# Optimization experiments

Measured on AMD Instinct MI355X. Metric: run time of the kernel, lower is better.

## Reference

```python
import jax, jax.numpy as jnp
import numpy as np

N_NODES = 50000
N_EDGES = 1_600_000
NUM_GRAPHS = 64
F_NODE = 32
F_EDGE = 16
H = 64
L = 3
BN_EPS = 1e-5


def setup_inputs() -> dict:
    key = jax.random.key(0)
    ks = jax.random.split(key, 20)
    x = jax.random.normal(ks[0], (N_NODES, F_NODE), jnp.float32)
    edge_attr = jax.random.normal(ks[1], (N_EDGES, F_EDGE), jnp.float32)
    edge_index = jax.random.randint(ks[2], (2, N_EDGES), 0, N_NODES, dtype=jnp.int64)
    batch = jnp.sort(jax.random.randint(ks[3], (N_NODES,), 0, NUM_GRAPHS, dtype=jnp.int64))

    def lin(k, fan_in, shape):
        return jax.random.normal(k, shape, jnp.float32) * (1.0 / np.sqrt(fan_in))

    node_W = lin(ks[4], F_NODE, (F_NODE, H));  node_b = jnp.zeros((H,), jnp.float32)
    edge_W = lin(ks[5], F_EDGE, (F_EDGE, H));  edge_b = jnp.zeros((H,), jnp.float32)
    # GINE per-layer MLP: Linear(H, 2H) -> ReLU -> Linear(2H, H)
    W1s = lin(ks[6], H, (L, H, 2 * H));   b1s = jnp.zeros((L, 2 * H), jnp.float32)
    W2s = lin(ks[7], 2 * H, (L, 2 * H, H)); b2s = jnp.zeros((L, H), jnp.float32)
    gammas = jnp.ones((L, H), jnp.float32)
    betas = jnp.zeros((L, H), jnp.float32)
    lin_W = lin(ks[8], H, (H, 1));  lin_b = jnp.zeros((1,), jnp.float32)
    return {
        "x": x, "edge_attr": edge_attr, "edge_index": edge_index, "batch": batch,
        "node_W": node_W, "node_b": node_b, "edge_W": edge_W, "edge_b": edge_b,
        "W1s": W1s, "b1s": b1s, "W2s": W2s, "b2s": b2s,
        "gammas": gammas, "betas": betas, "lin_W": lin_W, "lin_b": lin_b,
    }


def reference(x, edge_attr, edge_index, batch, node_W, node_b, edge_W, edge_b,
              W1s, b1s, W2s, b2s, gammas, betas, lin_W, lin_b):
    # node / edge embeddings
    h = x @ node_W + node_b                  # [N, H]
    e = edge_attr @ edge_W + edge_b          # [E, H]
    src, dst = edge_index[0], edge_index[1]
    for l in range(L):
        # GINEConv (eps=0): m_ij = relu(x_j + e_ij), aggregate sum at target
        m = jax.nn.relu(h[src] + e)                                  # [E, H]
        agg = jax.ops.segment_sum(m, dst, num_segments=N_NODES)     # [N, H]
        z = h + agg
        z = jax.nn.relu(z @ W1s[l] + b1s[l]) @ W2s[l] + b2s[l]       # GINE MLP
        # BatchNorm (training-mode batch stats, biased variance) + ReLU
        mu = jnp.mean(z, axis=0)
        var = jnp.var(z, axis=0)
        h = jax.nn.relu(gammas[l] * (z - mu) * jax.lax.rsqrt(var + BN_EPS) + betas[l])
    # global mean pool per graph
    counts = jax.ops.segment_sum(jnp.ones((N_NODES,), h.dtype), batch, num_segments=NUM_GRAPHS)
    gsum = jax.ops.segment_sum(h, batch, num_segments=NUM_GRAPHS)   # [G, H]
    graph_x = gsum / jnp.maximum(counts, 1.0)[:, None]
    return graph_x @ lin_W + lin_b                                   # [G, 1]
```

## Files before the change

kernel.cpp:

```cpp
#include <hip/hip_runtime.h>

#define NN 50000
#define NE 1600000
#define NG 64
#define HD 64
#define BN_EPS 1e-5f
#define NTILES ((NN + 31) / 32)
#define NBUCK 8
#define NPB 6250
#define NBINS (NBUCK * NN)
#define NEP (NE + 512)
#define SLOTS 3584

typedef unsigned short ushort_t;
typedef unsigned int uint_t;
typedef __attribute__((ext_vector_type(8))) short bf16x8;
typedef __attribute__((ext_vector_type(4))) float f32x4;

__device__ __forceinline__ float b2f(ushort_t u) {
  union { uint_t i; float f; } v; v.i = ((uint_t)u) << 16; return v.f;
}
__device__ __forceinline__ ushort_t f2b(float f) {
  union { float f; uint_t i; } v; v.f = f;
  uint_t x = v.i;
  return (ushort_t)((x + 0x7fffu + ((x >> 16) & 1u)) >> 16);
}
__device__ __forceinline__ uint_t packsplit(float f) {
  ushort_t hi = f2b(f);
  float r = f - b2f(hi);
  ushort_t lo = f2b(r);
  return (uint_t)hi | ((uint_t)lo << 16);
}
__device__ __forceinline__ float LDF(const void* p, int i, int isb) {
  return isb ? b2f(((const ushort_t*)p)[i]) : ((const float*)p)[i];
}
__device__ __forceinline__ int LDI(const void* p, int i, int is64) {
  return is64 ? ((const int*)p)[2 * i] : ((const int*)p)[i];
}
__device__ __forceinline__ int clampi(int v, int hi) {
  return (v < 0) ? 0 : (v >= hi ? hi - 1 : v);
}

__global__ void detect_k(const uint_t* __restrict__ xw, const uint_t* __restrict__ ew,
                         int* __restrict__ flags) {
  int t = threadIdx.x;
  uint_t w = xw[t];
  uint_t b = (w >> 8) & 0x7fu;
  unsigned long long m1 = __ballot(b >= 0x3au && b <= 0x42u);
  unsigned long long m2 = __ballot(ew[2 * t + 1] == 0u);
  if (t == 0) {
    flags[0] = (__popcll(m1) >= 32) ? 1 : 0;
    flags[1] = (__popcll(m2) >= 56) ? 1 : 0;
  }
}

__global__ void __launch_bounds__(256) node_embed(
    const void* __restrict__ x, const void* __restrict__ W,
    const void* __restrict__ b, float* __restrict__ h, const int* __restrict__ flags) {
  __shared__ float xs[64 * 32];
  int isb = flags[0];
  int t = threadIdx.x;
  int base = blockIdx.x * 64;
  int nodes = NN - base; if (nodes > 64) nodes = 64;
  int idx = t * 8;
  if (idx < nodes * 32) {
    if (isb) {
      const uint4* p = (const uint4*)((const ushort_t*)x + base * 32);
      uint4 u = p[t];
      ushort_t* pu = (ushort_t*)&u;
      #pragma unroll
      for (int q = 0; q < 8; q++) xs[idx + q] = b2f(pu[q]);
    } else {
      const float4* p = (const float4*)((const float*)x + base * 32);
      float4 a = p[2 * t], d = p[2 * t + 1];
      xs[idx + 0] = a.x; xs[idx + 1] = a.y; xs[idx + 2] = a.z; xs[idx + 3] = a.w;
      xs[idx + 4] = d.x; xs[idx + 5] = d.y; xs[idx + 6] = d.z; xs[idx + 7] = d.w;
    }
  }
  int c = t & 63, s0 = t >> 6;
  float w[32];
  #pragma unroll
  for (int k = 0; k < 32; k++) w[k] = LDF(W, k * 64 + c, isb);
  float bc = LDF(b, c, isb);
  __syncthreads();
  #pragma unroll 4
  for (int i = 0; i < 16; i++) {
    int slot = s0 * 16 + i;
    int node = base + slot;
    if (node < NN) {
      float acc = bc;
      #pragma unroll
      for (int k = 0; k < 32; k++) acc += xs[slot * 32 + k] * w[k];
      h[node * 64 + c] = acc;
    }
  }
}

__global__ void __launch_bounds__(256) hist_k(
    const void* __restrict__ eidx, int* __restrict__ hist, const int* __restrict__ flags) {
  int is64 = flags[1];
  int e = blockIdx.x * 256 + threadIdx.x;
  if (e >= NE) return;
  int d = clampi(LDI(eidx, NE + e, is64), NN);
  int s = clampi(LDI(eidx, e, is64), NN);
  int bin = (s / NPB) * NN + d;
  atomicAdd(&hist[bin], 1);
}

__global__ void __launch_bounds__(1024) scan_k(
    const int* __restrict__ hist, int* __restrict__ starts, int* __restrict__ meta) {
  __shared__ int buf[1024];
  __shared__ int sA[NBUCK + 1];
  __shared__ int sT[NBUCK];
  __shared__ int sPT[NBUCK];
  int t = threadIdx.x;
  int active = t < 1000;
  const int4* h4 = (const int4*)hist;
  int4* s4 = (int4*)starts;
  int ssum = 0;
  if (active) {
    for (int i = t * 100; i < t * 100 + 100; i++) {
      int4 v = h4[i];
      ssum += v.x + v.y + v.z + v.w;
    }
  }
  buf[t] = ssum;
  __syncthreads();
  if (t < NBUCK) {
    int T = 0;
    for (int i = t * 125; i < t * 125 + 125; i++) T += buf[i];
    sT[t] = T;
  }
  __syncthreads();
  if (t == 0) {
    int a = 0, pt = 0;
    for (int b = 0; b < NBUCK; b++) {
      sA[b] = a; sPT[b] = pt;
      meta[b] = a;
      meta[16 + b] = a + sT[b];
      pt += sT[b];
      a = (a + sT[b] + 63) & ~63;
    }
    sA[NBUCK] = a;
    meta[NBUCK] = a;
  }
  __syncthreads();
  for (int d = 1; d < 1024; d <<= 1) {
    int x = (t >= d) ? buf[t - d] : 0;
    __syncthreads();
    buf[t] += x;
    __syncthreads();
  }
  if (active) {
    int b = t / 125;
    int run = sA[b] + (buf[t] - ssum - sPT[b]);
    for (int i = t * 100; i < t * 100 + 100; i++) {
      int4 v = h4[i];
      int4 o;
      o.x = run; run += v.x;
      o.y = run; run += v.y;
      o.z = run; run += v.z;
      o.w = run; run += v.w;
      s4[i] = o;
    }
  }
}

__global__ void pad_fill(const int* __restrict__ meta, int* __restrict__ perm,
                         int* __restrict__ psrc, int* __restrict__ pdst) {
  int t = threadIdx.x;
  for (int b = 0; b < NBUCK; b++) {
    int re = meta[16 + b], ae = meta[b + 1];
    for (int p = re + t; p < ae; p += 64) {
      perm[p] = 0; psrc[p] = 0; pdst[p] = NN;
    }
  }
}

__global__ void __launch_bounds__(256) scatter_k(
    const void* __restrict__ eidx, int* __restrict__ cursor,
    int* __restrict__ perm, int* __restrict__ psrc, int* __restrict__ pdst,
    const int* __restrict__ flags) {
  int is64 = flags[1];
  int e = blockIdx.x * 256 + threadIdx.x;
  if (e >= NE) return;
  int d = clampi(LDI(eidx, NE + e, is64), NN);
  int s = clampi(LDI(eidx, e, is64), NN);
  int bin = (s / NPB) * NN + d;
  int pos = atomicAdd(&cursor[bin], 1);
  perm[pos] = e;
  psrc[pos] = s;
  pdst[pos] = d;
}

__global__ void __launch_bounds__(256) pack_eattr(
    const void* __restrict__ eattr, const int* __restrict__ perm,
    ushort_t* __restrict__ phi, ushort_t* __restrict__ plo,
    const int* __restrict__ flags, const int* __restrict__ meta) {
  int isb = flags[0];
  int pos = blockIdx.x * 256 + threadIdx.x;
  if (pos >= meta[8]) return;
  int e = perm[pos];
  int tile = pos >> 4, r = pos & 15;
  union U8 { ushort_t s[8]; uint4 u; };
  if (isb) {
    const uint4* p = (const uint4*)((const ushort_t*)eattr + (size_t)e * 16);
    uint4 h0 = p[0], h1 = p[1];
    ((uint4*)phi)[tile * 32 + r] = h0;
    ((uint4*)phi)[tile * 32 + 16 + r] = h1;
  } else {
    const float4* p = (const float4*)((const float*)eattr + (size_t)e * 16);
    U8 hi[2], lo[2];
    #pragma unroll
    for (int q = 0; q < 4; q++) {
      float4 v = p[q];
      float vv[4] = {v.x, v.y, v.z, v.w};
      #pragma unroll
      for (int j = 0; j < 4; j++) {
        int idx = q * 4 + j;
        ushort_t hb = f2b(vv[j]);
        hi[idx >> 3].s[idx & 7] = hb;
        lo[idx >> 3].s[idx & 7] = f2b(vv[j] - b2f(hb));
      }
    }
    ((uint4*)phi)[tile * 32 + r] = hi[0].u;
    ((uint4*)phi)[tile * 32 + 16 + r] = hi[1].u;
    ((uint4*)plo)[tile * 32 + r] = lo[0].u;
    ((uint4*)plo)[tile * 32 + 16 + r] = lo[1].u;
  }
}

__global__ void __launch_bounds__(256) edge_mfma(
    const ushort_t* __restrict__ phi, const ushort_t* __restrict__ plo,
    const int* __restrict__ psrc, const int* __restrict__ pdst,
    const uint4* __restrict__ wfrag, const float* __restrict__ h,
    float* __restrict__ agg, const int* __restrict__ flags,
    const int* __restrict__ meta) {
  __shared__ float es[64 * 68];
  __shared__ int ss[64], sd[64];
  int A[9];
  #pragma unroll
  for (int b = 0; b < 9; b++) A[b] = meta[b];
  int maxcb = 0;
  #pragma unroll
  for (int b = 0; b < NBUCK; b++) {
    int cb = (A[b + 1] - A[b]) >> 6;
    maxcb = cb > maxcb ? cb : maxcb;
  }
  int chunk;
  if (maxcb <= SLOTS) {
    int xcd = blockIdx.x & 7, s = blockIdx.x >> 3;
    if (s >= ((A[xcd + 1] - A[xcd]) >> 6)) return;
    chunk = (A[xcd] >> 6) + s;
  } else {
    chunk = blockIdx.x;
    if (chunk * 64 >= A[8]) return;
  }
  int base = chunk * 64;
  int isb = flags[0];
  int t = threadIdx.x;
  if (t < 64) ss[t] = psrc[base + t];
  else if (t < 128) sd[t - 64] = pdst[base + t - 64];
  int w = t >> 6, lane = t & 63, kg = lane >> 4, cr = lane & 15;
  int tile = chunk * 4 + w;
  union FR { uint4 u; bf16x8 v; };
  FR ahi, alo;
  ahi.u = make_uint4(0u, 0u, 0u, 0u);
  alo.u = ahi.u;
  if (kg < 2) {
    ahi.u = ((const uint4*)phi)[tile * 32 + kg * 16 + cr];
    if (!isb) alo.u = ((const uint4*)plo)[tile * 32 + kg * 16 + cr];
  }
  f32x4 acc[4];
  #pragma unroll
  for (int nt = 0; nt < 4; nt++) acc[nt] = (f32x4){0.f, 0.f, 0.f, 0.f};
  #pragma unroll
  for (int nt = 0; nt < 4; nt++) {
    FR bh; bh.u = wfrag[nt * 64 + lane];
    acc[nt] = __builtin_amdgcn_mfma_f32_16x16x32_bf16(ahi.v, bh.v, acc[nt], 0, 0, 0);
    if (!isb) {
      FR bl; bl.u = wfrag[256 + nt * 64 + lane];
      acc[nt] = __builtin_amdgcn_mfma_f32_16x16x32_bf16(ahi.v, bl.v, acc[nt], 0, 0, 0);
      acc[nt] = __builtin_amdgcn_mfma_f32_16x16x32_bf16(alo.v, bh.v, acc[nt], 0, 0, 0);
    }
  }
  const float* ebias = (const float*)(wfrag + 512);
  #pragma unroll
  for (int nt = 0; nt < 4; nt++) {
    float bv = ebias[nt * 16 + cr];
    #pragma unroll
    for (int r = 0; r < 4; r++)
      es[(w * 16 + kg * 4 + r) * 68 + nt * 16 + cr] = acc[nt][r] + bv;
  }
  __syncthreads();
  int c = lane, s0 = w;
  float hv[16];
  #pragma unroll
  for (int i = 0; i < 16; i++)
    hv[i] = h[(size_t)ss[s0 * 16 + i] * 64 + c];
  float accr = 0.f;
  int cur = -1;
  #pragma unroll
  for (int i = 0; i < 16; i++) {
    int slot = s0 * 16 + i;
    int dn = sd[slot];
    float m = hv[i] + es[slot * 68 + c];
    m = m > 0.f ? m : 0.f;
    if (dn != cur) {
      if (cur >= 0 && cur < NN) atomicAdd(&agg[cur * 64 + c], accr);
      cur = dn; accr = 0.f;
    }
    accr += m;
  }
  if (cur >= 0 && cur < NN) atomicAdd(&agg[cur * 64 + c], accr);
}

__global__ void __launch_bounds__(256) edge_sorted(
    const void* __restrict__ eattr, const int* __restrict__ perm,
    const int* __restrict__ psrc, const int* __restrict__ pdst,
    const void* __restrict__ eW, const void* __restrict__ eb,
    const float* __restrict__ h, float* __restrict__ agg,
    const int* __restrict__ flags, const int* __restrict__ meta) {
  __shared__ float ea[64 * 16];
  __shared__ int ss[64], sd[64];
  int isb = flags[0];
  int t = threadIdx.x;
  int base = blockIdx.x * 64;
  if (base >= meta[8]) return;
  if (t < 64) ss[t] = psrc[base + t];
  else if (t < 128) sd[t - 64] = pdst[base + t - 64];
  {
    int slot = t >> 2, q = t & 3;
    int pe = perm[base + slot];
    if (isb) {
      const uint2* p = (const uint2*)((const ushort_t*)eattr + (size_t)pe * 16 + q * 4);
      uint2 u = *p;
      ea[slot * 16 + q * 4 + 0] = b2f((ushort_t)(u.x & 0xffffu));
      ea[slot * 16 + q * 4 + 1] = b2f((ushort_t)(u.x >> 16));
      ea[slot * 16 + q * 4 + 2] = b2f((ushort_t)(u.y & 0xffffu));
      ea[slot * 16 + q * 4 + 3] = b2f((ushort_t)(u.y >> 16));
    } else {
      const float4* p = (const float4*)((const float*)eattr + (size_t)pe * 16 + q * 4);
      float4 v = *p;
      ea[slot * 16 + q * 4 + 0] = v.x;
      ea[slot * 16 + q * 4 + 1] = v.y;
      ea[slot * 16 + q * 4 + 2] = v.z;
      ea[slot * 16 + q * 4 + 3] = v.w;
    }
  }
  int c = t & 63, s0 = t >> 6;
  float w[16];
  #pragma unroll
  for (int k = 0; k < 16; k++) w[k] = LDF(eW, k * 64 + c, isb);
  float bc = LDF(eb, c, isb);
  __syncthreads();
  float acc = 0.f;
  int cur = -1;
  for (int i = 0; i < 16; i++) {
    int slot = s0 * 16 + i;
    int sn = ss[slot], dn = sd[slot];
    float e = bc;
    #pragma unroll
    for (int k = 0; k < 16; k++) e += ea[slot * 16 + k] * w[k];
    float m = h[sn * 64 + c] + e;
    m = m > 0.f ? m : 0.f;
    if (dn != cur) {
      if (cur >= 0 && cur < NN) atomicAdd(&agg[cur * 64 + c], acc);
      cur = dn; acc = 0.f;
    }
    acc += m;
  }
  if (cur >= 0 && cur < NN) atomicAdd(&agg[cur * 64 + c], acc);
}

__global__ void __launch_bounds__(256) prep_w(
    const void* __restrict__ W1s, const void* __restrict__ W2s,
    const void* __restrict__ eW, const void* __restrict__ eB,
    uint4* __restrict__ wpk, const int* __restrict__ flags) {
  int l = blockIdx.x, t = threadIdx.x, isb = flags[0];
  union U8 { ushort_t s[8]; uint4 u; };
  if (l == 3) {
    uint4* wfrag = wpk + 3 * 4096;
    int nt = t >> 6, lane = t & 63;
    int col = nt * 16 + (lane & 15);
    U8 hi, lo;
    #pragma unroll
    for (int j = 0; j < 8; j++) {
      int k = (lane >> 4) * 8 + j;
      float wf = (k < 16) ? LDF(eW, k * 64 + col, isb) : 0.f;
      ushort_t hb = f2b(wf);
      hi.s[j] = hb;
      lo.s[j] = f2b(wf - b2f(hb));
    }
    wfrag[nt * 64 + lane] = hi.u;
    wfrag[256 + nt * 64 + lane] = lo.u;
    if (t < 64) ((float*)(wfrag + 512))[t] = LDF(eB, t, isb);
    return;
  }
  uint4* w1hi = wpk + (size_t)l * 4096;
  uint4* w1lo = w1hi + 1024;
  uint4* w2hi = w1hi + 2048;
  uint4* w2lo = w1hi + 3072;
  for (int o = t; o < 1024; o += 256) {
    int lane = o & 63, f = (o >> 6) & 7, hh = o >> 9;
    int q = lane >> 4, m = lane & 15;
    {
      int kc = f >> 2, i = f & 3;
      U8 hi, lo;
      #pragma unroll
      for (int j = 0; j < 8; j++) {
        int idx = l * 8192 + (kc * 32 + q * 8 + j) * 128 + (hh * 4 + i) * 16 + m;
        float wf = LDF(W1s, idx, isb);
        ushort_t hb = f2b(wf);
        hi.s[j] = hb;
        lo.s[j] = f2b(wf - b2f(hb));
      }
      w1hi[o] = hi.u;
      w1lo[o] = lo.u;
    }
    {
      int kc = f >> 1, i = f & 1;
      U8 hi, lo;
      #pragma unroll
      for (int j = 0; j < 8; j++) {
        int idx = l * 8192 + (kc * 32 + q * 8 + j) * 64 + (hh * 2 + i) * 16 + m;
        float wf = LDF(W2s, idx, isb);
        ushort_t hb = f2b(wf);
        hi.s[j] = hb;
        lo.s[j] = f2b(wf - b2f(hb));
      }
      w2hi[o] = hi.u;
      w2lo[o] = lo.u;
    }
  }
}

__global__ void __launch_bounds__(256) mlp_mfma(
    const float* __restrict__ h, const float* agg,
    const uint4* __restrict__ wpk, const void* __restrict__ b1s,
    const void* __restrict__ b2s,
    float* z2out, float* __restrict__ bnsum, const int* __restrict__ flags, int layer) {
  __shared__ uint_t zs[32 * 65];
  __shared__ uint_t a1s[32 * 129];
  int isb = flags[0];
  int t = threadIdx.x;
  int w = t >> 6, lane = t & 63, q = lane >> 4, m = lane & 15;
  int mt = w & 1;
  int hh = w >> 1;
  int ng1 = hh * 4;
  int ng2 = hh * 2;
  int b1off = layer * 128, b2off = layer * 64;
  const uint4* w1hi = wpk + (size_t)layer * 4096;
  const uint4* w1lo = w1hi + 1024;
  const uint4* w2hi = w1hi + 2048;
  const uint4* w2lo = w1hi + 3072;

  union FR { uint4 u; bf16x8 v; };
  FR w1f[4][2], w2f[2][4];
  #pragma unroll
  for (int kc = 0; kc < 2; kc++)
    #pragma unroll
    for (int i = 0; i < 4; i++)
      w1f[i][kc].u = w1hi[(hh * 8 + kc * 4 + i) * 64 + lane];
  #pragma unroll
  for (int kc = 0; kc < 4; kc++)
    #pragma unroll
    for (int i = 0; i < 2; i++)
      w2f[i][kc].u = w2hi[(hh * 8 + kc * 2 + i) * 64 + lane];

  float b1v[4], b2v[2];
  #pragma unroll
  for (int i = 0; i < 4; i++) b1v[i] = LDF(b1s, b1off + (ng1 + i) * 16 + m, isb);
  #pragma unroll
  for (int i = 0; i < 2; i++) b2v[i] = LDF(b2s, b2off + (ng2 + i) * 16 + m, isb);

  int srow = t >> 3, scol = (t & 7) * 8;
  float ps[2] = {0.f, 0.f}, pq[2] = {0.f, 0.f};

  for (int tile = blockIdx.x; tile < NTILES; tile += gridDim.x) {
    int base = tile * 32;
    __syncthreads();
    {
      int gr = base + srow;
      if (gr < NN) {
        const float4* hp = (const float4*)(h + (size_t)gr * 64 + scol);
        const float4* ap = (const float4*)(agg + (size_t)gr * 64 + scol);
        float4 h0 = hp[0], h1 = hp[1], a0 = ap[0], a1 = ap[1];
        zs[srow * 65 + scol + 0] = packsplit(h0.x + a0.x);
        zs[srow * 65 + scol + 1] = packsplit(h0.y + a0.y);
        zs[srow * 65 + scol + 2] = packsplit(h0.z + a0.z);
        zs[srow * 65 + scol + 3] = packsplit(h0.w + a0.w);
        zs[srow * 65 + scol + 4] = packsplit(h1.x + a1.x);
        zs[srow * 65 + scol + 5] = packsplit(h1.y + a1.y);
        zs[srow * 65 + scol + 6] = packsplit(h1.z + a1.z);
        zs[srow * 65 + scol + 7] = packsplit(h1.w + a1.w);
      } else {
        #pragma unroll
        for (int jj = 0; jj < 8; jj++) zs[srow * 65 + scol + jj] = 0;
      }
    }
    __syncthreads();
    f32x4 acc1[4];
    #pragma unroll
    for (int i = 0; i < 4; i++) acc1[i] = (f32x4){0.f, 0.f, 0.f, 0.f};
    #pragma unroll
    for (int kc = 0; kc < 2; kc++) {
      int ab = (mt * 16 + m) * 65 + kc * 32 + q * 8;
      bf16x8 ahi, alo;
      #pragma unroll
      for (int j = 0; j < 8; j++) {
        uint_t u = zs[ab + j];
        ahi[j] = (short)(u & 0xffffu);
        alo[j] = (short)(u >> 16);
      }
      #pragma unroll
      for (int i = 0; i < 4; i++) {
        acc1[i] = __builtin_amdgcn_mfma_f32_16x16x32_bf16(ahi, w1f[i][kc].v, acc1[i], 0, 0, 0);
        acc1[i] = __builtin_amdgcn_mfma_f32_16x16x32_bf16(alo, w1f[i][kc].v, acc1[i], 0, 0, 0);
        if (!isb) {
          FR bl;
          bl.u = w1lo[(hh * 8 + kc * 4 + i) * 64 + lane];
          acc1[i] = __builtin_amdgcn_mfma_f32_16x16x32_bf16(ahi, bl.v, acc1[i], 0, 0, 0);
        }
      }
    }
    #pragma unroll
    for (int i = 0; i < 4; i++) {
      #pragma unroll
      for (int r = 0; r < 4; r++) {
        float v = acc1[i][r] + b1v[i];
        v = v > 0.f ? v : 0.f;
        a1s[(mt * 16 + q * 4 + r) * 129 + (ng1 + i) * 16 + m] = packsplit(v);
      }
    }
    __syncthreads();
    f32x4 acc2[2];
    #pragma unroll
    for (int i = 0; i < 2; i++) acc2[i] = (f32x4){0.f, 0.f, 0.f, 0.f};
    #pragma unroll
    for (int kc = 0; kc < 4; kc++) {
      int ab = (mt * 16 + m) * 129 + kc * 32 + q * 8;
      bf16x8 ahi, alo;
      #pragma unroll
      for (int j = 0; j < 8; j++) {
        uint_t u = a1s[ab + j];
        ahi[j] = (short)(u & 0xffffu);
        alo[j] = (short)(u >> 16);
      }
      #pragma unroll
      for (int i = 0; i < 2; i++) {
        acc2[i] = __builtin_amdgcn_mfma_f32_16x16x32_bf16(ahi, w2f[i][kc].v, acc2[i], 0, 0, 0);
        acc2[i] = __builtin_amdgcn_mfma_f32_16x16x32_bf16(alo, w2f[i][kc].v, acc2[i], 0, 0, 0);
        if (!isb) {
          FR bl;
          bl.u = w2lo[(hh * 8 + kc * 2 + i) * 64 + lane];
          acc2[i] = __builtin_amdgcn_mfma_f32_16x16x32_bf16(ahi, bl.v, acc2[i], 0, 0, 0);
        }
      }
    }
    #pragma unroll
    for (int i = 0; i < 2; i++) {
      int col = (ng2 + i) * 16 + m;
      #pragma unroll
      for (int r = 0; r < 4; r++) {
        int gr = base + mt * 16 + q * 4 + r;
        if (gr < NN) {
          float v = acc2[i][r] + b2v[i];
          z2out[(size_t)gr * 64 + col] = v;
          ps[i] += v; pq[i] += v * v;
        }
      }
    }
  }
  __syncthreads();
  float* red = (float*)zs;
  if (t < 128) red[t] = 0.f;
  __syncthreads();
  #pragma unroll
  for (int i = 0; i < 2; i++) {
    int col = (ng2 + i) * 16 + m;
    atomicAdd(&red[col], ps[i]);
    atomicAdd(&red[64 + col], pq[i]);
  }
  __syncthreads();
  if (t < 128) atomicAdd(&bnsum[t], red[t]);
}

__global__ void bn_fin(const float* __restrict__ bnsum, const void* __restrict__ gammas,
                       const void* __restrict__ betas, float* __restrict__ scsh,
                       const int* __restrict__ flags, int layer) {
  int c = threadIdx.x;
  int isb = flags[0];
  float inv_n = 1.0f / (float)NN;
  float mu = bnsum[c] * inv_n;
  float var = bnsum[64 + c] * inv_n - mu * mu;
  var = var > 0.f ? var : 0.f;
  float sc = LDF(gammas, layer * 64 + c, isb) * rsqrtf(var + BN_EPS);
  scsh[c] = sc;
  scsh[64 + c] = LDF(betas, layer * 64 + c, isb) - mu * sc;
}

__global__ void __launch_bounds__(256) bn_apply(
    const float* __restrict__ z2, const float* __restrict__ scsh, float* __restrict__ h) {
  int t = blockIdx.x * 256 + threadIdx.x;
  if (t < NN * 16) {
    float4 z = ((const float4*)z2)[t];
    int c4 = t & 15;
    float4 sc = ((const float4*)scsh)[c4];
    float4 sh = ((const float4*)(scsh + 64))[c4];
    float4 r;
    r.x = fmaxf(z.x * sc.x + sh.x, 0.f);
    r.y = fmaxf(z.y * sc.y + sh.y, 0.f);
    r.z = fmaxf(z.z * sc.z + sh.z, 0.f);
    r.w = fmaxf(z.w * sc.w + sh.w, 0.f);
    ((float4*)h)[t] = r;
  }
}

__global__ void __launch_bounds__(256) find_bounds(
    const void* __restrict__ batch, int* __restrict__ bounds, const int* __restrict__ flags) {
  int is64 = flags[1];
  int i = blockIdx.x * 256 + threadIdx.x;
  if (i >= NN) return;
  int cur = clampi(LDI(batch, i, is64), NG);
  if (i == 0) {
    for (int g = 0; g <= cur; g++) bounds[g] = 0;
  } else {
    int prev = clampi(LDI(batch, i - 1, is64), NG);
    for (int g = prev + 1; g <= cur; g++) bounds[g] = i;
  }
  if (i == NN - 1) {
    for (int g = cur + 1; g <= NG; g++) bounds[g] = NN;
  }
}

__global__ void __launch_bounds__(256) pool_final(
    const float* __restrict__ h, const int* __restrict__ bounds,
    const void* __restrict__ linW, const void* __restrict__ linB,
    float* __restrict__ out, const int* __restrict__ flags) {
  __shared__ float red[4][64];
  int isb = flags[0];
  int g = blockIdx.x;
  int t = threadIdx.x, c = t & 63, w = t >> 6;
  int s = bounds[g], e = bounds[g + 1];
  float acc = 0.f;
  for (int i = s + w; i < e; i += 4) acc += h[i * 64 + c];
  red[w][c] = acc;
  __syncthreads();
  if (t < 64) {
    float v = red[0][c] + red[1][c] + red[2][c] + red[3][c];
    float cnt = (float)(e - s); if (cnt < 1.f) cnt = 1.f;
    v = (v / cnt) * LDF(linW, c, isb);
    #pragma unroll
    for (int m = 32; m >= 1; m >>= 1) v += __shfl_xor(v, m, 64);
    if (c == 0) out[g] = v + LDF(linB, 0, isb);
  }
}

extern "C" void kernel_launch(void* const* d_in, const int* in_sizes, int n_in,
                              void* d_out, int out_size, void* d_ws, size_t ws_size,
                              hipStream_t stream) {
  const void* x     = d_in[0];
  const void* eattr = d_in[1];
  const void* eidx  = d_in[2];
  const void* batch = d_in[3];
  const void* nodeW = d_in[4];
  const void* nodeB = d_in[5];
  const void* edgeW = d_in[6];
  const void* edgeB = d_in[7];
  const void* W1s   = d_in[8];
  const void* b1s   = d_in[9];
  const void* W2s   = d_in[10];
  const void* b2s   = d_in[11];
  const void* gam   = d_in[12];
  const void* bet   = d_in[13];
  const void* linW  = d_in[14];
  const void* linB  = d_in[15];
  float* out = (float*)d_out;

  int*   flags  = (int*)d_ws;
  int*   meta   = flags + 16;
  float* h      = (float*)(meta + 48);
  float* agg    = h + (size_t)NN * HD;
  float* bnsum  = agg + (size_t)NN * HD;
  float* scsh   = bnsum + 128;
  int*   bounds = (int*)(scsh + 128);
  int*   offs   = bounds + 80;
  int*   cursor = offs + NBINS;
  int*   perm   = cursor + NBINS;
  int*   psrc   = perm + NEP;
  int*   pdst   = psrc + NEP;

  size_t base_words = 64ull + 2ull * NN * HD + 128 + 128 + 80
                    + 2ull * NBINS + 3ull * NEP;
  size_t wpk_words_start = (base_words + 3ull) & ~3ull;
  size_t wpk_words = (3ull * 4096 + 528) * 4;
  size_t needed = (wpk_words_start + wpk_words) * 4ull;
  if (ws_size < needed) return;
  uint4* wpk = (uint4*)((float*)d_ws + wpk_words_start);
  uint4* wfrag = wpk + 3ull * 4096;
  size_t z2_start = wpk_words_start + wpk_words;
  float* z2sep = (float*)d_ws + z2_start;
  int have_z2 = ws_size >= (z2_start + (size_t)NN * HD) * 4ull;
  float* z2 = have_z2 ? z2sep : agg;
  size_t pat_start = z2_start + (size_t)NN * HD;
  size_t pat_words = (size_t)NEP * 8;
  int have_pat = have_z2 && (ws_size >= (pat_start + 2ull * pat_words) * 4ull);
  ushort_t* phi = (ushort_t*)((float*)d_ws + pat_start);
  ushort_t* plo = (ushort_t*)((float*)d_ws + pat_start + pat_words);

  detect_k<<<1, 64, 0, stream>>>((const uint_t*)x, (const uint_t*)eidx, flags);
  prep_w<<<4, 256, 0, stream>>>(W1s, W2s, edgeW, edgeB, wpk, flags);
  node_embed<<<(NN + 63) / 64, 256, 0, stream>>>(x, nodeW, nodeB, h, flags);

  hipMemsetAsync(offs, 0, (size_t)NBINS * sizeof(int), stream);
  hist_k<<<NE / 256, 256, 0, stream>>>(eidx, offs, flags);
  scan_k<<<1, 1024, 0, stream>>>(offs, cursor, meta);
  pad_fill<<<1, 64, 0, stream>>>(meta, perm, psrc, pdst);
  scatter_k<<<NE / 256, 256, 0, stream>>>(eidx, cursor, perm, psrc, pdst, flags);
  if (have_pat)
    pack_eattr<<<NEP / 256, 256, 0, stream>>>(eattr, perm, phi, plo, flags, meta);

  for (int l = 0; l < 3; l++) {
    hipMemsetAsync(agg, 0, (size_t)NN * HD * sizeof(float), stream);
    if (have_pat)
      edge_mfma<<<8 * SLOTS, 256, 0, stream>>>(phi, plo, psrc, pdst, wfrag, h, agg, flags, meta);
    else
      edge_sorted<<<NEP / 64, 256, 0, stream>>>(eattr, perm, psrc, pdst, edgeW, edgeB, h, agg, flags, meta);
    hipMemsetAsync(bnsum, 0, 128 * sizeof(int), stream);
    mlp_mfma<<<784, 256, 0, stream>>>(h, agg, wpk, b1s, b2s, z2, bnsum, flags, l);
    bn_fin<<<1, 64, 0, stream>>>(bnsum, gam, bet, scsh, flags, l);
    bn_apply<<<3125, 256, 0, stream>>>(z2, scsh, h);
  }
  find_bounds<<<(NN + 255) / 256, 256, 0, stream>>>(batch, bounds, flags);
  pool_final<<<NG, 256, 0, stream>>>(h, bounds, linW, linB, out, flags);
}
```

Measured before the change: 1.099 ms.

## Replace single-block histogram scan with three-phase multi-block scan

The exclusive scan over 400K histogram bins ran in one 1024-thread block, with each thread serially walking 100 int4 values. It is now split into a per-chunk reduction (200 blocks), a small single-block pass that computes per-chunk bases and bucket metadata, and a per-chunk scan that writes the start offsets. This spreads a latency-bound serial kernel across the whole GPU at the cost of two extra launches and a second read of the histogram.

```diff
diff --git a/kernel.cpp b/kernel.cpp
--- a/kernel.cpp
+++ b/kernel.cpp
@@ -11,6 +11,9 @@
 #define NBINS (NBUCK * NN)
 #define NEP (NE + 512)
 #define SLOTS 3584
+#define CHUNK 2000
+#define NCHUNK (NBINS / CHUNK)
+#define CPB (NCHUNK / NBUCK)
 
 typedef unsigned short ushort_t;
 typedef unsigned int uint_t;
@@ -107,62 +110,90 @@
   atomicAdd(&hist[bin], 1);
 }
 
-__global__ void __launch_bounds__(1024) scan_k(
-    const int* __restrict__ hist, int* __restrict__ starts, int* __restrict__ meta) {
-  __shared__ int buf[1024];
+__global__ void __launch_bounds__(256) scan_a(
+    const int* __restrict__ hist, int* __restrict__ csum) {
+  __shared__ int red[256];
+  int c = blockIdx.x, t = threadIdx.x;
+  int s = 0;
+  if (t < 250) {
+    const int4* h4 = (const int4*)(hist + c * CHUNK) + t * 2;
+    int4 a = h4[0], b = h4[1];
+    s = a.x + a.y + a.z + a.w + b.x + b.y + b.z + b.w;
+  }
+  red[t] = s;
+  __syncthreads();
+  for (int d = 128; d > 0; d >>= 1) {
+    if (t < d) red[t] += red[t + d];
+    __syncthreads();
+  }
+  if (t == 0) csum[c] = red[0];
+}
+
+__global__ void __launch_bounds__(256) scan_b(
+    const int* __restrict__ csum, int* __restrict__ cbase, int* __restrict__ meta) {
+  __shared__ int sc[NCHUNK];
+  __shared__ int sT[NBUCK];
   __shared__ int sA[NBUCK + 1];
-  __shared__ int sT[NBUCK];
-  __shared__ int sPT[NBUCK];
   int t = threadIdx.x;
-  int active = t < 1000;
-  const int4* h4 = (const int4*)hist;
-  int4* s4 = (int4*)starts;
-  int ssum = 0;
-  if (active) {
-    for (int i = t * 100; i < t * 100 + 100; i++) {
-      int4 v = h4[i];
-      ssum += v.x + v.y + v.z + v.w;
-    }
-  }
-  buf[t] = ssum;
+  if (t < NCHUNK) sc[t] = csum[t];
   __syncthreads();
   if (t < NBUCK) {
     int T = 0;
-    for (int i = t * 125; i < t * 125 + 125; i++) T += buf[i];
+    for (int i = 0; i < CPB; i++) T += sc[t * CPB + i];
     sT[t] = T;
   }
   __syncthreads();
   if (t == 0) {
-    int a = 0, pt = 0;
+    int a = 0;
     for (int b = 0; b < NBUCK; b++) {
-      sA[b] = a; sPT[b] = pt;
+      sA[b] = a;
       meta[b] = a;
       meta[16 + b] = a + sT[b];
-      pt += sT[b];
       a = (a + sT[b] + 63) & ~63;
     }
+    meta[NBUCK] = a;
     sA[NBUCK] = a;
-    meta[NBUCK] = a;
-  }
-  __syncthreads();
-  for (int d = 1; d < 1024; d <<= 1) {
+  }
+  __syncthreads();
+  if (t < NBUCK) {
+    int run = sA[t];
+    for (int i = 0; i < CPB; i++) { cbase[t * CPB + i] = run; run += sc[t * CPB + i]; }
+  }
+}
+
+__global__ void __launch_bounds__(256) scan_c(
+    const int* __restrict__ hist, const int* __restrict__ cbase,
+    int* __restrict__ starts) {
+  __shared__ int buf[256];
+  int c = blockIdx.x, t = threadIdx.x;
+  int4 a = {0, 0, 0, 0}, b = {0, 0, 0, 0};
+  int s = 0;
+  if (t < 250) {
+    const int4* h4 = (const int4*)(hist + c * CHUNK) + t * 2;
+    a = h4[0]; b = h4[1];
+    s = a.x + a.y + a.z + a.w + b.x + b.y + b.z + b.w;
+  }
+  buf[t] = s;
+  __syncthreads();
+  for (int d = 1; d < 256; d <<= 1) {
     int x = (t >= d) ? buf[t - d] : 0;
     __syncthreads();
     buf[t] += x;
     __syncthreads();
   }
-  if (active) {
-    int b = t / 125;
-    int run = sA[b] + (buf[t] - ssum - sPT[b]);
-    for (int i = t * 100; i < t * 100 + 100; i++) {
-      int4 v = h4[i];
-      int4 o;
-      o.x = run; run += v.x;
-      o.y = run; run += v.y;
-      o.z = run; run += v.z;
-      o.w = run; run += v.w;
-      s4[i] = o;
-    }
+  if (t < 250) {
+    int run = cbase[c] + buf[t] - s;
+    int4 o1, o2;
+    o1.x = run; run += a.x;
+    o1.y = run; run += a.y;
+    o1.z = run; run += a.z;
+    o1.w = run; run += a.w;
+    o2.x = run; run += b.x;
+    o2.y = run; run += b.y;
+    o2.z = run; run += b.z;
+    o2.w = run; run += b.w;
+    int4* s4 = (int4*)(starts + c * CHUNK) + t * 2;
+    s4[0] = o1; s4[1] = o2;
   }
 }
 
@@ -685,14 +716,16 @@
   float* bnsum  = agg + (size_t)NN * HD;
   float* scsh   = bnsum + 128;
   int*   bounds = (int*)(scsh + 128);
-  int*   offs   = bounds + 80;
+  int*   csum   = bounds + 80;
+  int*   cbase  = csum + NCHUNK;
+  int*   offs   = cbase + NCHUNK;
   int*   cursor = offs + NBINS;
   int*   perm   = cursor + NBINS;
   int*   psrc   = perm + NEP;
   int*   pdst   = psrc + NEP;
 
   size_t base_words = 64ull + 2ull * NN * HD + 128 + 128 + 80
-                    + 2ull * NBINS + 3ull * NEP;
+                    + 2ull * NCHUNK + 2ull * NBINS + 3ull * NEP;
   size_t wpk_words_start = (base_words + 3ull) & ~3ull;
   size_t wpk_words = (3ull * 4096 + 528) * 4;
   size_t needed = (wpk_words_start + wpk_words) * 4ull;
@@ -715,7 +748,9 @@
 
   hipMemsetAsync(offs, 0, (size_t)NBINS * sizeof(int), stream);
   hist_k<<<NE / 256, 256, 0, stream>>>(eidx, offs, flags);
-  scan_k<<<1, 1024, 0, stream>>>(offs, cursor, meta);
+  scan_a<<<NCHUNK, 256, 0, stream>>>(offs, csum);
+  scan_b<<<1, 256, 0, stream>>>(csum, cbase, meta);
+  scan_c<<<NCHUNK, 256, 0, stream>>>(offs, cbase, cursor);
   pad_fill<<<1, 64, 0, stream>>>(meta, perm, psrc, pdst);
   scatter_k<<<NE / 256, 256, 0, stream>>>(eidx, cursor, perm, psrc, pdst, flags);
   if (have_pat)
```

Result: faster. 948.8 us (-13.7%).
